# Kernel tuning notes

Measured on AMD Instinct MI355X. Metric: run time of the kernel, lower is better.

Reference implementation:

```python
import jax, jax.numpy as jnp
import numpy as np

ROW_LO, ROW_HI = 19, 67   # SELECTED_ROWS = range(19, 67) -> 48 rows
NBITS = 22
OUT_BITS = 506            # (7 + 7 + 9) groups * 22 bits


def setup_inputs() -> dict:
    key = jax.random.key(0)
    k1, k2 = jax.random.split(key)
    # CSI input [B, 2, 126, 128], values in [0, 1) like the normalized dataset
    x = jax.random.uniform(k1, (16, 2, 126, 128), dtype=jnp.float32)
    # codebook: K entries of shape [2, 48, 8]; the module's second pass uses 1-codebook,
    # giving an effective 2K-entry codebook, exactly as forward() does.
    codebook = jax.random.uniform(k2, (32768, 2, 48, 8), dtype=jnp.float32)
    return {"x": x, "codebook": codebook}


def _forward(x, codebook):
    B = x.shape[0]
    # select rows 19..66 and split last dim 128 -> 16*8
    xs = x[:, :, ROW_LO:ROW_HI].reshape(B, 2, ROW_HI - ROW_LO, 16, 8)  # [B,2,48,16,8]
    # effective codebook = [data ; 1 - data]  (the two subtract passes in forward)
    full = jnp.concatenate([codebook, 1.0 - codebook], axis=0)  # [2K,2,48,8]
    # squared distance summed over dims (2,48), codebook broadcast over the 16 axis:
    # d[a,k,i,j] = sum_pq (xs[a,p,q,i,j] - full[k,p,q,j])^2
    # expand quadratic form to avoid materializing [B,2K,2,48,16,8]
    xsq = jnp.sum(xs * xs, axis=(1, 2))          # [B,16,8]
    csq = jnp.sum(full * full, axis=(1, 2))      # [2K,8]
    cross = jnp.einsum('apqij,kpqj->akij', xs, full)  # [B,2K,16,8]
    d = xsq[:, None] - 2.0 * cross + csq[None, :, None, :]  # [B,2K,16,8]
    # three argmin groups over the 2K codebook axis
    s1 = d[:, :, :7, :4].sum(-1)   # [B,2K,7]
    s2 = d[:, :, :7, 4:].sum(-1)   # [B,2K,7]
    s3 = d[:, :, 7:, :].sum(-1)    # [B,2K,9]
    i1 = jnp.argmin(s1, axis=1).astype(jnp.int32)  # [B,7]
    i2 = jnp.argmin(s2, axis=1).astype(jnp.int32)  # [B,7]
    i3 = jnp.argmin(s3, axis=1).astype(jnp.int32)  # [B,9]
    ints = jnp.concatenate([i1, i2, i3], axis=1)   # [B,23]
    # little-endian bit extraction: output[:,:,a] = idx % 2; idx //= 2
    bits = (ints[..., None] >> jnp.arange(NBITS, dtype=jnp.int32)) & 1  # [B,23,22]
    bits = bits.reshape(B, OUT_BITS).astype(jnp.float32)
    return jnp.concatenate([jnp.zeros((B, 6), jnp.float32), bits], axis=1)  # [B,512]


def reference(x, codebook):
    return _forward(x, codebook)
```

## Files before the change

### kernel.cpp

```cpp
#include <hip/hip_runtime.h>
#include <stdint.h>

typedef unsigned long long u64;
typedef unsigned int u32;
typedef __attribute__((ext_vector_type(8))) short bf16x8;
typedef __attribute__((ext_vector_type(4))) float f32x4;

__device__ __forceinline__ u64 fkey(float f, unsigned idx) {
    unsigned u = __float_as_uint(f);
    u = (u & 0x80000000u) ? ~u : (u | 0x80000000u);
    return ((u64)u << 32) | (u64)idx;
}
__device__ __forceinline__ u64 umin64(u64 a, u64 b) { return a < b ? a : b; }
__device__ __forceinline__ unsigned short f2bf(float f) {
    unsigned u = __float_as_uint(f);
    return (unsigned short)((u + 0x7FFFu + ((u >> 16) & 1u)) >> 16);
}
__device__ __forceinline__ float bf2f(unsigned short b) {
    return __uint_as_float((unsigned)b << 16);
}

extern "C" __global__ __launch_bounds__(256)
void prep_kernel(const float* __restrict__ x, unsigned short* __restrict__ Xs,
                 float* __restrict__ xsum, u64* __restrict__ sb) {
    __shared__ float xbuf[768];
    const int row = blockIdx.x;
    const int a = row >> 4, i = row & 15;
    for (int pass = 0; pass < 3; ++pass) {
        int t = pass * 256 + threadIdx.x;
        int g = t >> 3, j = t & 7;
        int p = g / 48, q = g - 48 * p;
        float v = x[((size_t)(a * 2 + p) * 126 + (19 + q)) * 128 + (i * 8 + j)];
        xbuf[t] = v;
        unsigned short b1 = f2bf(v);
        unsigned short b2 = f2bf(v - bf2f(b1));
        int par = (j >> 2);
        int colin = g * 4 + (j & 3);
        int c = colin >> 5;
        int col64 = par * 32 + (colin & 31);
        size_t base = (size_t)row * 1536 + c * 64 + col64;
        Xs[base] = b1;
        Xs[base + 768] = b2;
    }
    __syncthreads();
    if (threadIdx.x < 2) {
        int off = threadIdx.x ? 4 : 0;
        float s = 0.f;
        for (int g = 0; g < 96; ++g)
            for (int j = 0; j < 4; ++j)
                s += xbuf[g * 8 + off + j];
        xsum[threadIdx.x * 256 + row] = s;
    }
    if (row == 0) {
        for (int t = threadIdx.x; t < 368; t += 256) sb[t] = ~0ULL;
    }
}

extern "C" __global__ __launch_bounds__(512, 4)
void gemm_kernel(const float* __restrict__ cb, const unsigned short* __restrict__ Xs,
                 const float* __restrict__ xsum, u64* __restrict__ sb) {
    __shared__ __align__(16) unsigned short cbt[128][64];
    __shared__ __align__(16) unsigned short xst[512][64];

    const int tid = threadIdx.x;
    const int lane = tid & 63;
    const int wid = tid >> 6;
    const int k0 = blockIdx.x * 64;
    const int eb = (wid & 1) * 32;
    const int rb = (wid >> 1) * 64;
    const int l15 = lane & 15;
    const int g4 = lane >> 4;
    const int h7 = lane & 7;

    const int se = tid >> 4;
    const int sgl = (tid >> 1) & 7;
    const int shalf = tid & 1;
    const int scol = shalf * 32 + sgl * 4;
    const int ssw = (((scol >> 3) ^ (se & 7)) << 3) + (sgl & 1) * 4;

    const int gswz = h7 ^ (lane >> 3);

    f32x4 acc[2][2][4] = {};
    float sp0 = 0.f, sq0 = 0.f, sp1 = 0.f, sq1 = 0.f;

    for (int c = 0; c < 12; ++c) {
        __syncthreads();
        const float* s1 = cb + (size_t)(k0 + se) * 768 + (c * 8 + sgl) * 8 + shalf * 4;
        float4 v1 = *(const float4*)s1;
        float4 v2 = *(const float4*)(s1 + 32 * 768);
        sp0 += v1.x + v1.y + v1.z + v1.w;
        sq0 += v1.x * v1.x + v1.y * v1.y + v1.z * v1.z + v1.w * v1.w;
        sp1 += v2.x + v2.y + v2.z + v2.w;
        sq1 += v2.x * v2.x + v2.y * v2.y + v2.z * v2.z + v2.w * v2.w;
        unsigned short a1x = f2bf(v1.x), a1y = f2bf(v1.y), a1z = f2bf(v1.z), a1w = f2bf(v1.w);
        unsigned short a2x = f2bf(v2.x), a2y = f2bf(v2.y), a2z = f2bf(v2.z), a2w = f2bf(v2.w);
        ushort4 c1a = make_ushort4(a1x, a1y, a1z, a1w);
        ushort4 c1b = make_ushort4(f2bf(v1.x - bf2f(a1x)), f2bf(v1.y - bf2f(a1y)),
                                   f2bf(v1.z - bf2f(a1z)), f2bf(v1.w - bf2f(a1w)));
        ushort4 c2a = make_ushort4(a2x, a2y, a2z, a2w);
        ushort4 c2b = make_ushort4(f2bf(v2.x - bf2f(a2x)), f2bf(v2.y - bf2f(a2y)),
                                   f2bf(v2.z - bf2f(a2z)), f2bf(v2.w - bf2f(a2w)));
        *(ushort4*)&cbt[se][ssw]      = c1a;
        *(ushort4*)&cbt[se + 64][ssw] = c1b;
        *(ushort4*)&cbt[se + 32][ssw] = c2a;
        *(ushort4*)&cbt[se + 96][ssw] = c2b;
#pragma unroll
        for (int i = 0; i < 8; ++i) {
            int row = (wid << 6) + (i << 3) + (lane >> 3);
            const unsigned short* gs = Xs + (size_t)(row & 255) * 1536 + (row >> 8) * 768
                                          + c * 64 + gswz * 8;
            __builtin_amdgcn_global_load_lds(
                (const __attribute__((address_space(1))) u32*)gs,
                (__attribute__((address_space(3))) u32*)&xst[(wid << 6) + (i << 3)][0],
                16, 0, 0);
        }
        __syncthreads();
#pragma unroll
        for (int par = 0; par < 2; ++par) {
            const int sws = ((((par << 2) | g4) ^ h7) << 3);
            bf16x8 A1[2], A2[2];
#pragma unroll
            for (int m = 0; m < 2; ++m) {
                A1[m] = *(const bf16x8*)&cbt[eb + m * 16 + l15][sws];
                A2[m] = *(const bf16x8*)&cbt[eb + m * 16 + l15 + 64][sws];
            }
#pragma unroll
            for (int n = 0; n < 4; ++n) {
                const unsigned short* xr = &xst[rb + n * 16 + l15][sws];
                bf16x8 B1 = *(const bf16x8*)xr;
                bf16x8 B2 = *(const bf16x8*)(xr + 256 * 64);
#pragma unroll
                for (int m = 0; m < 2; ++m) {
                    acc[par][m][n] = __builtin_amdgcn_mfma_f32_16x16x32_bf16(A1[m], B1, acc[par][m][n], 0, 0, 0);
                    acc[par][m][n] = __builtin_amdgcn_mfma_f32_16x16x32_bf16(A2[m], B1, acc[par][m][n], 0, 0, 0);
                    acc[par][m][n] = __builtin_amdgcn_mfma_f32_16x16x32_bf16(A1[m], B2, acc[par][m][n], 0, 0, 0);
                    acc[par][m][n] = __builtin_amdgcn_mfma_f32_16x16x32_bf16(A2[m], B2, acc[par][m][n], 0, 0, 0);
                }
            }
        }
    }

#pragma unroll
    for (int m = 2; m <= 8; m <<= 1) {
        sp0 += __shfl_xor(sp0, m); sq0 += __shfl_xor(sq0, m);
        sp1 += __shfl_xor(sp1, m); sq1 += __shfl_xor(sq1, m);
    }
    __syncthreads();
    float* stf = (float*)&cbt[0][0];
    u64* msb = (u64*)((char*)&cbt[0][0] + 1024);
    if ((tid & 15) < 2) {
        int par = tid & 1, e = tid >> 4;
        stf[par * 128 + e]           = sp0;
        stf[par * 128 + 64 + e]      = sq0;
        stf[par * 128 + e + 32]      = sp1;
        stf[par * 128 + 64 + e + 32] = sq1;
    }
    if (tid < 368) msb[tid] = ~0ULL;
    __syncthreads();

#pragma unroll
    for (int n = 0; n < 4; ++n) {
        const int r = rb + n * 16 + l15;
        const float xl = xsum[r], xh = xsum[256 + r];
        u64 kA = ~0ULL, kB = ~0ULL;
#pragma unroll
        for (int m = 0; m < 2; ++m) {
#pragma unroll
            for (int reg = 0; reg < 4; ++reg) {
                const int el = eb + m * 16 + (g4 << 2) + reg;
                const unsigned kg = (unsigned)(k0 + el);
                float stl = stf[el],       sql = stf[64 + el];
                float sth = stf[128 + el], sqh = stf[192 + el];
                float dl = acc[0][m][n][reg], dh = acc[1][m][n][reg];
                float lo_d = sql - 2.f * dl;
                float lo_m = (384.f - 2.f * stl + sql) - 2.f * (xl - dl);
                float hi_d = sqh - 2.f * dh;
                float hi_m = (384.f - 2.f * sth + sqh) - 2.f * (xh - dh);
                if (l15 < 7) {
                    kA = umin64(kA, umin64(fkey(lo_d, kg), fkey(lo_m, kg + 32768u)));
                    kB = umin64(kB, umin64(fkey(hi_d, kg), fkey(hi_m, kg + 32768u)));
                } else {
                    kA = umin64(kA, umin64(fkey(lo_d + hi_d, kg), fkey(lo_m + hi_m, kg + 32768u)));
                }
            }
        }
        kA = umin64(kA, __shfl_xor(kA, 16));
        kA = umin64(kA, __shfl_xor(kA, 32));
        kB = umin64(kB, __shfl_xor(kB, 16));
        kB = umin64(kB, __shfl_xor(kB, 32));
        if (lane < 16) {
            int a_ = r >> 4;
            if (l15 < 7) {
                atomicMin(&msb[a_ * 23 + l15], kA);
                atomicMin(&msb[a_ * 23 + 7 + l15], kB);
            } else {
                atomicMin(&msb[a_ * 23 + 14 + (l15 - 7)], kA);
            }
        }
    }
    __syncthreads();
    if (tid < 368) atomicMin(&sb[tid], msb[tid]);
}

extern "C" __global__ __launch_bounds__(512)
void bits_kernel(const u64* __restrict__ sb, float* __restrict__ out) {
    const int a = blockIdx.x;
    const int pos = threadIdx.x;
    float v = 0.f;
    if (pos >= 6) {
        int b = pos - 6;
        int s = b / 22;
        int bb = b - s * 22;
        unsigned idx = (unsigned)(sb[a * 23 + s] & 0xFFFFFFFFu);
        v = (float)((idx >> bb) & 1u);
    }
    out[a * 512 + pos] = v;
}

extern "C" void kernel_launch(void* const* d_in, const int* in_sizes, int n_in,
                              void* d_out, int out_size, void* d_ws, size_t ws_size,
                              hipStream_t stream) {
    const float* x  = (const float*)d_in[0];
    const float* cb = (const float*)d_in[1];
    char* ws = (char*)d_ws;
    unsigned short* Xs = (unsigned short*)ws;
    float* xsum        = (float*)(ws + 786432);
    u64*   sb          = (u64*)(ws + 788480);
    float* out = (float*)d_out;

    prep_kernel<<<256, 256, 0, stream>>>(x, Xs, xsum, sb);
    gemm_kernel<<<512, 512, 0, stream>>>(cb, Xs, xsum, sb);
    bits_kernel<<<16, 512, 0, stream>>>(sb, out);
}
```

Measured before the change: 69.82 us.

## Double-buffer codebook and X tiles in LDS to overlap loads with MFMA

The GEMM main loop now keeps two LDS buffers for the codebook split tiles and the X tiles. It prefetches chunk c+1 (global codebook loads and async global_load_lds for X) while MFMAs run on chunk c, then splits and stores the next codebook tile afterwards, so each iteration needs one barrier instead of two. The MFMA section also raises wave priority with s_setprio. The cost is twice the LDS (about 160KB versus 80KB), and occupancy drops to 2 blocks/CU, which lowers latency hiding across blocks.

```diff
diff --git a/kernel.cpp b/kernel.cpp
--- a/kernel.cpp
+++ b/kernel.cpp
@@ -56,11 +56,11 @@
     }
 }
 
-extern "C" __global__ __launch_bounds__(512, 4)
+extern "C" __global__ __launch_bounds__(512, 2)
 void gemm_kernel(const float* __restrict__ cb, const unsigned short* __restrict__ Xs,
                  const float* __restrict__ xsum, u64* __restrict__ sb) {
-    __shared__ __align__(16) unsigned short cbt[128][64];
-    __shared__ __align__(16) unsigned short xst[512][64];
+    __shared__ __align__(16) unsigned short cbt[2][128][64];
+    __shared__ __align__(16) unsigned short xst[2][512][64];
 
     const int tid = threadIdx.x;
     const int lane = tid & 63;
@@ -82,12 +82,14 @@
 
     f32x4 acc[2][2][4] = {};
     float sp0 = 0.f, sq0 = 0.f, sp1 = 0.f, sq1 = 0.f;
-
-    for (int c = 0; c < 12; ++c) {
-        __syncthreads();
+    float4 v1, v2;
+
+    auto load_cb = [&](int c) {
         const float* s1 = cb + (size_t)(k0 + se) * 768 + (c * 8 + sgl) * 8 + shalf * 4;
-        float4 v1 = *(const float4*)s1;
-        float4 v2 = *(const float4*)(s1 + 32 * 768);
+        v1 = *(const float4*)s1;
+        v2 = *(const float4*)(s1 + 32 * 768);
+    };
+    auto split_cb = [&](int buf) {
         sp0 += v1.x + v1.y + v1.z + v1.w;
         sq0 += v1.x * v1.x + v1.y * v1.y + v1.z * v1.z + v1.w * v1.w;
         sp1 += v2.x + v2.y + v2.z + v2.w;
@@ -100,10 +102,12 @@
         ushort4 c2a = make_ushort4(a2x, a2y, a2z, a2w);
         ushort4 c2b = make_ushort4(f2bf(v2.x - bf2f(a2x)), f2bf(v2.y - bf2f(a2y)),
                                    f2bf(v2.z - bf2f(a2z)), f2bf(v2.w - bf2f(a2w)));
-        *(ushort4*)&cbt[se][ssw]      = c1a;
-        *(ushort4*)&cbt[se + 64][ssw] = c1b;
-        *(ushort4*)&cbt[se + 32][ssw] = c2a;
-        *(ushort4*)&cbt[se + 96][ssw] = c2b;
+        *(ushort4*)&cbt[buf][se][ssw]      = c1a;
+        *(ushort4*)&cbt[buf][se + 64][ssw] = c1b;
+        *(ushort4*)&cbt[buf][se + 32][ssw] = c2a;
+        *(ushort4*)&cbt[buf][se + 96][ssw] = c2b;
+    };
+    auto issue_x = [&](int buf, int c) {
 #pragma unroll
         for (int i = 0; i < 8; ++i) {
             int row = (wid << 6) + (i << 3) + (lane >> 3);
@@ -111,22 +115,35 @@
                                           + c * 64 + gswz * 8;
             __builtin_amdgcn_global_load_lds(
                 (const __attribute__((address_space(1))) u32*)gs,
-                (__attribute__((address_space(3))) u32*)&xst[(wid << 6) + (i << 3)][0],
+                (__attribute__((address_space(3))) u32*)&xst[buf][(wid << 6) + (i << 3)][0],
                 16, 0, 0);
         }
-        __syncthreads();
+    };
+
+    load_cb(0);
+    split_cb(0);
+    issue_x(0, 0);
+    __syncthreads();
+
+    for (int c = 0; c < 12; ++c) {
+        const int cur = c & 1, nxt = cur ^ 1;
+        if (c < 11) {
+            load_cb(c + 1);
+            issue_x(nxt, c + 1);
+        }
+        __builtin_amdgcn_s_setprio(1);
 #pragma unroll
         for (int par = 0; par < 2; ++par) {
             const int sws = ((((par << 2) | g4) ^ h7) << 3);
             bf16x8 A1[2], A2[2];
 #pragma unroll
             for (int m = 0; m < 2; ++m) {
-                A1[m] = *(const bf16x8*)&cbt[eb + m * 16 + l15][sws];
-                A2[m] = *(const bf16x8*)&cbt[eb + m * 16 + l15 + 64][sws];
+                A1[m] = *(const bf16x8*)&cbt[cur][eb + m * 16 + l15][sws];
+                A2[m] = *(const bf16x8*)&cbt[cur][eb + m * 16 + l15 + 64][sws];
             }
 #pragma unroll
             for (int n = 0; n < 4; ++n) {
-                const unsigned short* xr = &xst[rb + n * 16 + l15][sws];
+                const unsigned short* xr = &xst[cur][rb + n * 16 + l15][sws];
                 bf16x8 B1 = *(const bf16x8*)xr;
                 bf16x8 B2 = *(const bf16x8*)(xr + 256 * 64);
 #pragma unroll
@@ -138,6 +155,9 @@
                 }
             }
         }
+        __builtin_amdgcn_s_setprio(0);
+        if (c < 11) split_cb(nxt);
+        __syncthreads();
     }
 
 #pragma unroll
@@ -145,9 +165,8 @@
         sp0 += __shfl_xor(sp0, m); sq0 += __shfl_xor(sq0, m);
         sp1 += __shfl_xor(sp1, m); sq1 += __shfl_xor(sq1, m);
     }
-    __syncthreads();
-    float* stf = (float*)&cbt[0][0];
-    u64* msb = (u64*)((char*)&cbt[0][0] + 1024);
+    float* stf = (float*)&cbt[0][0][0];
+    u64* msb = (u64*)((char*)&cbt[0][0][0] + 1024);
     if ((tid & 15) < 2) {
         int par = tid & 1, e = tid >> 4;
         stf[par * 128 + e]           = sp0;
```

Result: slower. 88.20 us (+26.3%).

## Switch GEMM to 32x32x16 MFMA tiles with 4 waves per block

Applied to the files above, without the earlier changes.

Replaces the 16x16x32 bf16 MFMA tiling with 32x32x16 instructions. Each wave now covers all 64 codebook entries of the block against 64 x-rows, and the block shrinks from 512 to 256 threads. Each thread stages four codebook rows per chunk and issues twice as many LDS-direct x loads, and the argmin epilogue is remapped to the 32x32 accumulator layout. The aim is fewer LDS fragment reads per MFMA and higher MFMA throughput, at the cost of more accumulator registers and possibly lower occupancy.

```diff
diff --git a/kernel.cpp b/kernel.cpp
--- a/kernel.cpp
+++ b/kernel.cpp
@@ -4,7 +4,7 @@
 typedef unsigned long long u64;
 typedef unsigned int u32;
 typedef __attribute__((ext_vector_type(8))) short bf16x8;
-typedef __attribute__((ext_vector_type(4))) float f32x4;
+typedef __attribute__((ext_vector_type(16))) float f32x16;
 
 __device__ __forceinline__ u64 fkey(float f, unsigned idx) {
     unsigned u = __float_as_uint(f);
@@ -56,7 +56,7 @@
     }
 }
 
-extern "C" __global__ __launch_bounds__(512, 4)
+extern "C" __global__ __launch_bounds__(256, 2)
 void gemm_kernel(const float* __restrict__ cb, const unsigned short* __restrict__ Xs,
                  const float* __restrict__ xsum, u64* __restrict__ sb) {
     __shared__ __align__(16) unsigned short cbt[128][64];
@@ -66,108 +66,129 @@
     const int lane = tid & 63;
     const int wid = tid >> 6;
     const int k0 = blockIdx.x * 64;
-    const int eb = (wid & 1) * 32;
-    const int rb = (wid >> 1) * 64;
-    const int l15 = lane & 15;
-    const int g4 = lane >> 4;
+    const int rb = wid * 64;
+    const int l31 = lane & 31;
+    const int l5 = lane >> 5;
     const int h7 = lane & 7;
 
-    const int se = tid >> 4;
+    const int se0 = tid >> 4;
     const int sgl = (tid >> 1) & 7;
     const int shalf = tid & 1;
-    const int scol = shalf * 32 + sgl * 4;
-    const int ssw = (((scol >> 3) ^ (se & 7)) << 3) + (sgl & 1) * 4;
+    const int ssw = (((shalf * 32 + sgl * 4) >> 3) ^ (se0 & 7)) * 8 + (sgl & 1) * 4;
 
     const int gswz = h7 ^ (lane >> 3);
 
-    f32x4 acc[2][2][4] = {};
-    float sp0 = 0.f, sq0 = 0.f, sp1 = 0.f, sq1 = 0.f;
+    f32x16 acc[2][2][2] = {};
+    float sp[4] = {0.f, 0.f, 0.f, 0.f};
+    float sq[4] = {0.f, 0.f, 0.f, 0.f};
 
     for (int c = 0; c < 12; ++c) {
         __syncthreads();
-        const float* s1 = cb + (size_t)(k0 + se) * 768 + (c * 8 + sgl) * 8 + shalf * 4;
-        float4 v1 = *(const float4*)s1;
-        float4 v2 = *(const float4*)(s1 + 32 * 768);
-        sp0 += v1.x + v1.y + v1.z + v1.w;
-        sq0 += v1.x * v1.x + v1.y * v1.y + v1.z * v1.z + v1.w * v1.w;
-        sp1 += v2.x + v2.y + v2.z + v2.w;
-        sq1 += v2.x * v2.x + v2.y * v2.y + v2.z * v2.z + v2.w * v2.w;
-        unsigned short a1x = f2bf(v1.x), a1y = f2bf(v1.y), a1z = f2bf(v1.z), a1w = f2bf(v1.w);
-        unsigned short a2x = f2bf(v2.x), a2y = f2bf(v2.y), a2z = f2bf(v2.z), a2w = f2bf(v2.w);
-        ushort4 c1a = make_ushort4(a1x, a1y, a1z, a1w);
-        ushort4 c1b = make_ushort4(f2bf(v1.x - bf2f(a1x)), f2bf(v1.y - bf2f(a1y)),
-                                   f2bf(v1.z - bf2f(a1z)), f2bf(v1.w - bf2f(a1w)));
-        ushort4 c2a = make_ushort4(a2x, a2y, a2z, a2w);
-        ushort4 c2b = make_ushort4(f2bf(v2.x - bf2f(a2x)), f2bf(v2.y - bf2f(a2y)),
-                                   f2bf(v2.z - bf2f(a2z)), f2bf(v2.w - bf2f(a2w)));
-        *(ushort4*)&cbt[se][ssw]      = c1a;
-        *(ushort4*)&cbt[se + 64][ssw] = c1b;
-        *(ushort4*)&cbt[se + 32][ssw] = c2a;
-        *(ushort4*)&cbt[se + 96][ssw] = c2b;
-#pragma unroll
-        for (int i = 0; i < 8; ++i) {
-            int row = (wid << 6) + (i << 3) + (lane >> 3);
-            const unsigned short* gs = Xs + (size_t)(row & 255) * 1536 + (row >> 8) * 768
-                                          + c * 64 + gswz * 8;
+        {
+            const float* s1 = cb + (size_t)(k0 + se0) * 768 + (c * 8 + sgl) * 8 + shalf * 4;
+            float4 v1 = *(const float4*)s1;
+            float4 v2 = *(const float4*)(s1 + 32 * 768);
+            float4 v3 = *(const float4*)(s1 + 16 * 768);
+            float4 v4 = *(const float4*)(s1 + 48 * 768);
+            sp[0] += v1.x + v1.y + v1.z + v1.w;
+            sq[0] += v1.x * v1.x + v1.y * v1.y + v1.z * v1.z + v1.w * v1.w;
+            sp[1] += v2.x + v2.y + v2.z + v2.w;
+            sq[1] += v2.x * v2.x + v2.y * v2.y + v2.z * v2.z + v2.w * v2.w;
+            sp[2] += v3.x + v3.y + v3.z + v3.w;
+            sq[2] += v3.x * v3.x + v3.y * v3.y + v3.z * v3.z + v3.w * v3.w;
+            sp[3] += v4.x + v4.y + v4.z + v4.w;
+            sq[3] += v4.x * v4.x + v4.y * v4.y + v4.z * v4.z + v4.w * v4.w;
+            unsigned short a1x = f2bf(v1.x), a1y = f2bf(v1.y), a1z = f2bf(v1.z), a1w = f2bf(v1.w);
+            unsigned short a2x = f2bf(v2.x), a2y = f2bf(v2.y), a2z = f2bf(v2.z), a2w = f2bf(v2.w);
+            unsigned short a3x = f2bf(v3.x), a3y = f2bf(v3.y), a3z = f2bf(v3.z), a3w = f2bf(v3.w);
+            unsigned short a4x = f2bf(v4.x), a4y = f2bf(v4.y), a4z = f2bf(v4.z), a4w = f2bf(v4.w);
+            *(ushort4*)&cbt[se0][ssw]       = make_ushort4(a1x, a1y, a1z, a1w);
+            *(ushort4*)&cbt[se0 + 64][ssw]  = make_ushort4(f2bf(v1.x - bf2f(a1x)), f2bf(v1.y - bf2f(a1y)),
+                                                           f2bf(v1.z - bf2f(a1z)), f2bf(v1.w - bf2f(a1w)));
+            *(ushort4*)&cbt[se0 + 32][ssw]  = make_ushort4(a2x, a2y, a2z, a2w);
+            *(ushort4*)&cbt[se0 + 96][ssw]  = make_ushort4(f2bf(v2.x - bf2f(a2x)), f2bf(v2.y - bf2f(a2y)),
+                                                           f2bf(v2.z - bf2f(a2z)), f2bf(v2.w - bf2f(a2w)));
+            *(ushort4*)&cbt[se0 + 16][ssw]  = make_ushort4(a3x, a3y, a3z, a3w);
+            *(ushort4*)&cbt[se0 + 80][ssw]  = make_ushort4(f2bf(v3.x - bf2f(a3x)), f2bf(v3.y - bf2f(a3y)),
+                                                           f2bf(v3.z - bf2f(a3z)), f2bf(v3.w - bf2f(a3w)));
+            *(ushort4*)&cbt[se0 + 48][ssw]  = make_ushort4(a4x, a4y, a4z, a4w);
+            *(ushort4*)&cbt[se0 + 112][ssw] = make_ushort4(f2bf(v4.x - bf2f(a4x)), f2bf(v4.y - bf2f(a4y)),
+                                                           f2bf(v4.z - bf2f(a4z)), f2bf(v4.w - bf2f(a4w)));
+        }
+#pragma unroll
+        for (int i = 0; i < 16; ++i) {
+            int lrow = (wid << 7) + (i << 3) + (lane >> 3);
+            const unsigned short* gs = Xs + (size_t)(lrow & 255) * 1536
+                                          + (lrow >> 8) * 768 + c * 64 + gswz * 8;
             __builtin_amdgcn_global_load_lds(
                 (const __attribute__((address_space(1))) u32*)gs,
-                (__attribute__((address_space(3))) u32*)&xst[(wid << 6) + (i << 3)][0],
+                (__attribute__((address_space(3))) u32*)&xst[(wid << 7) + (i << 3)][0],
                 16, 0, 0);
         }
         __syncthreads();
 #pragma unroll
         for (int par = 0; par < 2; ++par) {
-            const int sws = ((((par << 2) | g4) ^ h7) << 3);
-            bf16x8 A1[2], A2[2];
-#pragma unroll
-            for (int m = 0; m < 2; ++m) {
-                A1[m] = *(const bf16x8*)&cbt[eb + m * 16 + l15][sws];
-                A2[m] = *(const bf16x8*)&cbt[eb + m * 16 + l15 + 64][sws];
+#pragma unroll
+            for (int ks = 0; ks < 2; ++ks) {
+                const int sws = ((par * 4 + ks * 2 + l5) ^ h7) * 8;
+                bf16x8 A1[2], A2[2], B1[2], B2[2];
+#pragma unroll
+                for (int m = 0; m < 2; ++m) {
+                    A1[m] = *(const bf16x8*)&cbt[m * 32 + l31][sws];
+                    A2[m] = *(const bf16x8*)&cbt[m * 32 + l31 + 64][sws];
+                }
+#pragma unroll
+                for (int n = 0; n < 2; ++n) {
+                    B1[n] = *(const bf16x8*)&xst[rb + n * 32 + l31][sws];
+                    B2[n] = *(const bf16x8*)&xst[rb + n * 32 + l31 + 256][sws];
+                }
+#pragma unroll
+                for (int m = 0; m < 2; ++m)
+#pragma unroll
+                    for (int n = 0; n < 2; ++n) {
+                        acc[par][m][n] = __builtin_amdgcn_mfma_f32_32x32x16_bf16(A1[m], B1[n], acc[par][m][n], 0, 0, 0);
+                        acc[par][m][n] = __builtin_amdgcn_mfma_f32_32x32x16_bf16(A2[m], B1[n], acc[par][m][n], 0, 0, 0);
+                        acc[par][m][n] = __builtin_amdgcn_mfma_f32_32x32x16_bf16(A1[m], B2[n], acc[par][m][n], 0, 0, 0);
+                        acc[par][m][n] = __builtin_amdgcn_mfma_f32_32x32x16_bf16(A2[m], B2[n], acc[par][m][n], 0, 0, 0);
+                    }
             }
-#pragma unroll
-            for (int n = 0; n < 4; ++n) {
-                const unsigned short* xr = &xst[rb + n * 16 + l15][sws];
-                bf16x8 B1 = *(const bf16x8*)xr;
-                bf16x8 B2 = *(const bf16x8*)(xr + 256 * 64);
-#pragma unroll
-                for (int m = 0; m < 2; ++m) {
-                    acc[par][m][n] = __builtin_amdgcn_mfma_f32_16x16x32_bf16(A1[m], B1, acc[par][m][n], 0, 0, 0);
-                    acc[par][m][n] = __builtin_amdgcn_mfma_f32_16x16x32_bf16(A2[m], B1, acc[par][m][n], 0, 0, 0);
-                    acc[par][m][n] = __builtin_amdgcn_mfma_f32_16x16x32_bf16(A1[m], B2, acc[par][m][n], 0, 0, 0);
-                    acc[par][m][n] = __builtin_amdgcn_mfma_f32_16x16x32_bf16(A2[m], B2, acc[par][m][n], 0, 0, 0);
-                }
-            }
-        }
-    }
-
-#pragma unroll
-    for (int m = 2; m <= 8; m <<= 1) {
-        sp0 += __shfl_xor(sp0, m); sq0 += __shfl_xor(sq0, m);
-        sp1 += __shfl_xor(sp1, m); sq1 += __shfl_xor(sq1, m);
-    }
+        }
+    }
+
+#pragma unroll
+    for (int m = 2; m <= 8; m <<= 1)
+#pragma unroll
+        for (int s = 0; s < 4; ++s) {
+            sp[s] += __shfl_xor(sp[s], m);
+            sq[s] += __shfl_xor(sq[s], m);
+        }
     __syncthreads();
     float* stf = (float*)&cbt[0][0];
     u64* msb = (u64*)((char*)&cbt[0][0] + 1024);
     if ((tid & 15) < 2) {
-        int par = tid & 1, e = tid >> 4;
-        stf[par * 128 + e]           = sp0;
-        stf[par * 128 + 64 + e]      = sq0;
-        stf[par * 128 + e + 32]      = sp1;
-        stf[par * 128 + 64 + e + 32] = sq1;
-    }
-    if (tid < 368) msb[tid] = ~0ULL;
-    __syncthreads();
-
-#pragma unroll
-    for (int n = 0; n < 4; ++n) {
-        const int r = rb + n * 16 + l15;
+        const int p = tid & 1;
+        const int eo[4] = {0, 32, 16, 48};
+#pragma unroll
+        for (int s = 0; s < 4; ++s) {
+            stf[p * 128 + se0 + eo[s]]      = sp[s];
+            stf[p * 128 + 64 + se0 + eo[s]] = sq[s];
+        }
+    }
+    for (int t = tid; t < 368; t += 256) msb[t] = ~0ULL;
+    __syncthreads();
+
+#pragma unroll
+    for (int n = 0; n < 2; ++n) {
+        const int r = rb + n * 32 + l31;
+        const int i_ = r & 15;
+        const int a_ = r >> 4;
         const float xl = xsum[r], xh = xsum[256 + r];
         u64 kA = ~0ULL, kB = ~0ULL;
 #pragma unroll
         for (int m = 0; m < 2; ++m) {
 #pragma unroll
-            for (int reg = 0; reg < 4; ++reg) {
-                const int el = eb + m * 16 + (g4 << 2) + reg;
+            for (int reg = 0; reg < 16; ++reg) {
+                const int el = m * 32 + (reg & 3) + 8 * (reg >> 2) + 4 * l5;
                 const unsigned kg = (unsigned)(k0 + el);
                 float stl = stf[el],       sql = stf[64 + el];
                 float sth = stf[128 + el], sqh = stf[192 + el];
@@ -176,7 +197,7 @@
                 float lo_m = (384.f - 2.f * stl + sql) - 2.f * (xl - dl);
                 float hi_d = sqh - 2.f * dh;
                 float hi_m = (384.f - 2.f * sth + sqh) - 2.f * (xh - dh);
-                if (l15 < 7) {
+                if (i_ < 7) {
                     kA = umin64(kA, umin64(fkey(lo_d, kg), fkey(lo_m, kg + 32768u)));
                     kB = umin64(kB, umin64(fkey(hi_d, kg), fkey(hi_m, kg + 32768u)));
                 } else {
@@ -184,22 +205,19 @@
                 }
             }
         }
-        kA = umin64(kA, __shfl_xor(kA, 16));
         kA = umin64(kA, __shfl_xor(kA, 32));
-        kB = umin64(kB, __shfl_xor(kB, 16));
         kB = umin64(kB, __shfl_xor(kB, 32));
-        if (lane < 16) {
-            int a_ = r >> 4;
-            if (l15 < 7) {
-                atomicMin(&msb[a_ * 23 + l15], kA);
-                atomicMin(&msb[a_ * 23 + 7 + l15], kB);
+        if (lane < 32) {
+            if (i_ < 7) {
+                atomicMin(&msb[a_ * 23 + i_], kA);
+                atomicMin(&msb[a_ * 23 + 7 + i_], kB);
             } else {
-                atomicMin(&msb[a_ * 23 + 14 + (l15 - 7)], kA);
+                atomicMin(&msb[a_ * 23 + 14 + (i_ - 7)], kA);
             }
         }
     }
     __syncthreads();
-    if (tid < 368) atomicMin(&sb[tid], msb[tid]);
+    for (int t = tid; t < 368; t += 256) atomicMin(&sb[t], msb[t]);
 }
 
 extern "C" __global__ __launch_bounds__(512)
@@ -229,6 +247,6 @@
     float* out = (float*)d_out;
 
     prep_kernel<<<256, 256, 0, stream>>>(x, Xs, xsum, sb);
-    gemm_kernel<<<512, 512, 0, stream>>>(cb, Xs, xsum, sb);
+    gemm_kernel<<<512, 256, 0, stream>>>(cb, Xs, xsum, sb);
     bits_kernel<<<16, 512, 0, stream>>>(sb, out);
 }
```

Result: slower. 79.93 us (+14.5%).
